# Kernel tuning notes

Hardware: AMD Instinct MI355X
Metric: run time of the kernel (lower is better)

The kernel has to match this reference:

```python
import jax, jax.numpy as jnp
import numpy as np

N = 100_000   # nodes
D = 128       # in_channels
H = 128       # hidden_channels
O = 128       # out_channels
M = 3_200_000 # adjacency nnz (avg degree 32)
E = 200_000   # query edges
P = 500_000   # common-neighbor pairs (padded, all valid here)
COS_EPS = 1e-8
DEG_EPS = 1e-6


def setup_inputs() -> dict:
    key = jax.random.key(0)
    ks = jax.random.split(key, 12)
    x = jax.random.normal(ks[0], (N, D), jnp.float32)
    adj_row = jnp.sort(jax.random.randint(ks[1], (M,), 0, N, jnp.int32))
    adj_col = jax.random.randint(ks[2], (M,), 0, N, jnp.int32)
    edges = jax.random.randint(ks[3], (2, E), 0, N, jnp.int32)
    cn_edge_idx = jnp.sort(jax.random.randint(ks[4], (P,), 0, E, jnp.int32))
    cn_node = jax.random.randint(ks[5], (P,), 0, N, jnp.int32)
    cn_valid = jnp.ones((P,), jnp.bool_)
    # MLP params (Kaiming-ish scale)
    W1 = jax.random.normal(ks[6], (D, H), jnp.float32) / np.sqrt(D)
    b1 = jnp.zeros((H,), jnp.float32)
    W2 = jax.random.normal(ks[7], (H, H), jnp.float32) / np.sqrt(H)
    b2 = jnp.zeros((H,), jnp.float32)
    W3 = jax.random.normal(ks[8], (H, O), jnp.float32) / np.sqrt(H)
    b3 = jnp.zeros((O,), jnp.float32)
    return dict(x=x, adj_row=adj_row, adj_col=adj_col, edges=edges,
                cn_edge_idx=cn_edge_idx, cn_node=cn_node, cn_valid=cn_valid,
                W1=W1, b1=b1, W2=W2, b2=b2, W3=W3, b3=b3)


def _cosine(a, b):
    # torch.nn.CosineSimilarity: dot / max(||a||*||b||, eps)
    dot = jnp.sum(a * b, axis=-1)
    na = jnp.sqrt(jnp.sum(a * a, axis=-1))
    nb = jnp.sqrt(jnp.sum(b * b, axis=-1))
    return dot / jnp.maximum(na * nb, COS_EPS)


def reference(x, adj_row, adj_col, edges, cn_edge_idx, cn_node, cn_valid,
              W1, b1, W2, b2, W3, b3):
    # degrees = adj.sum(-1) + 1e-6 (binary adjacency values)
    ones = jnp.ones(adj_row.shape[0], x.dtype)
    deg = jax.ops.segment_sum(ones, adj_row, num_segments=N) + DEG_EPS
    # x = x + (adj @ x) / deg[:, None]
    agg = jax.ops.segment_sum(x[adj_col], adj_row, num_segments=N)
    h = x + agg / deg[:, None]
    # MLP (BatchNorms are unused in the original forward; dropout = inference)
    h = jax.nn.relu(h @ W1 + b1)
    h = jax.nn.relu(h @ W2 + b2)
    h = h @ W3 + b3                      # [N, O]
    # gather per common-neighbor pair: u = edges[0][e], v = edges[1][e], c = neighbor
    u = edges[0][cn_edge_idx]
    v = edges[1][cn_edge_idx]
    hu, hv, hc = h[u], h[v], h[cn_node]  # [P, O] each
    w = _cosine(hu, hc) * _cosine(hv, hc)
    w = jnp.where(cn_valid, w, jnp.zeros((), h.dtype))
    # sparse row-sum over neighbors per query edge
    scores = jax.ops.segment_sum(w, cn_edge_idx, num_segments=E)
    return jax.nn.sigmoid(scores)
```

## Files before the change

kernel.cpp:

```cpp
#include <hip/hip_runtime.h>
#include <math.h>

constexpr int N_NODES = 100000;
constexpr int DIM     = 128;
constexpr int M_NNZ   = 3200000;
constexpr int E_EDGES = 200000;
constexpr int P_PAIRS = 500000;
constexpr int W_ELEMS = 3 * DIM * DIM;

typedef _Float16 half8  __attribute__((ext_vector_type(8)));
typedef _Float16 half4t __attribute__((ext_vector_type(4)));
typedef _Float16 half2t __attribute__((ext_vector_type(2)));
typedef float    f32x4  __attribute__((ext_vector_type(4)));
typedef float    f32x2  __attribute__((ext_vector_type(2)));
typedef unsigned int u32x2 __attribute__((ext_vector_type(2)));

#if defined(__has_builtin)
#  if __has_builtin(__builtin_amdgcn_cvt_scalef32_pk8_f16_fp8)
#    define HAVE_PK8 1
#  endif
#endif
#ifndef HAVE_PK8
#  define HAVE_PK8 0
#endif

__device__ inline half8 fp8x8_to_h8(u32x2 d) {
#if HAVE_PK8
    return __builtin_amdgcn_cvt_scalef32_pk8_f16_fp8(d, 1.0f);
#else
    f32x2 p0 = __builtin_amdgcn_cvt_pk_f32_fp8(d[0], false);
    f32x2 p1 = __builtin_amdgcn_cvt_pk_f32_fp8(d[0], true);
    f32x2 p2 = __builtin_amdgcn_cvt_pk_f32_fp8(d[1], false);
    f32x2 p3 = __builtin_amdgcn_cvt_pk_f32_fp8(d[1], true);
    return half8{(_Float16)p0[0], (_Float16)p0[1], (_Float16)p1[0], (_Float16)p1[1],
                 (_Float16)p2[0], (_Float16)p2[1], (_Float16)p3[0], (_Float16)p3[1]};
#endif
}

__device__ inline void stage_weight(const _Float16* __restrict__ src,
                                    _Float16* __restrict__ dst) {
    const int tid = threadIdx.x;
    #pragma unroll
    for (int j = 0; j < 8; ++j) {
        const int gg  = j * 256 + tid;
        const int row = gg >> 4, g = gg & 15;
        *(half8*)(dst + (row << 7) + ((g ^ (row & 15)) << 3)) =
            *(const half8*)(src + gg * 8);
    }
}

__device__ inline half8 ldsw(const _Float16* __restrict__ w,
                             int row, int q, int t, int l16) {
    return *(const half8*)(w + (row << 7) + (((q + 4 * t) ^ l16) << 3));
}

__global__ void prep_kernel(
    const float* __restrict__ W1, const float* __restrict__ W2,
    const float* __restrict__ W3, _Float16* __restrict__ Wt,
    const int* __restrict__ adj_row, int* __restrict__ rs, int* __restrict__ re,
    float* __restrict__ out) {
    const int tid = blockIdx.x * blockDim.x + threadIdx.x;
    if (tid < W_ELEMS) {
        int m = tid >> 14, n = (tid >> 7) & 127, k = tid & 127;
        const float* W = (m == 0) ? W1 : (m == 1) ? W2 : W3;
        Wt[tid] = (_Float16)W[k * DIM + n];
        return;
    }
    if (tid < W_ELEMS + M_NNZ) {
        const int p = tid - W_ELEMS;
        const int v = adj_row[p];
        if (p == 0) {
            rs[v] = 0;
            for (int w = 0; w < v; ++w) { rs[w] = 0; re[w] = 0; }
        } else {
            int pv = adj_row[p - 1];
            if (pv != v) {
                re[pv] = p; rs[v] = p;
                for (int w = pv + 1; w < v; ++w) { rs[w] = p; re[w] = p; }
            }
        }
        if (p == M_NNZ - 1) {
            re[v] = M_NNZ;
            for (int w = v + 1; w < N_NODES; ++w) { rs[w] = M_NNZ; re[w] = M_NNZ; }
        }
        return;
    }
    if (tid < W_ELEMS + M_NNZ + E_EDGES) {
        out[tid - W_ELEMS - M_NNZ] = 0.f;
    }
}

__global__ __launch_bounds__(256) void gemm1_kernel(
    const float* __restrict__ x, const _Float16* __restrict__ Wt,
    _Float16* __restrict__ y, unsigned char* __restrict__ y8) {
    __shared__ __align__(16) _Float16 lw[16384];
    const int lane = threadIdx.x & 63;
    const int wave = threadIdx.x >> 6;
    const int q = lane >> 4, l16 = lane & 15;
    const int rBase = blockIdx.x * 128 + wave * 32;

    const int row0 = rBase + l16, row1 = rBase + 16 + l16;
    const int r0 = min(row0, N_NODES - 1), r1 = min(row1, N_NODES - 1);
    const float* Ap0 = x + (size_t)r0 * DIM + q * 8;
    const float* Ap1 = x + (size_t)r1 * DIM + q * 8;
    half8 a0[4], a1[4];
    #pragma unroll
    for (int t = 0; t < 4; ++t) {
        float4 u0 = *(const float4*)(Ap0 + t * 32);
        float4 u1 = *(const float4*)(Ap0 + t * 32 + 4);
        float4 w0 = *(const float4*)(Ap1 + t * 32);
        float4 w1 = *(const float4*)(Ap1 + t * 32 + 4);
        a0[t] = half8{(_Float16)u0.x, (_Float16)u0.y, (_Float16)u0.z, (_Float16)u0.w,
                      (_Float16)u1.x, (_Float16)u1.y, (_Float16)u1.z, (_Float16)u1.w};
        a1[t] = half8{(_Float16)w0.x, (_Float16)w0.y, (_Float16)w0.z, (_Float16)w0.w,
                      (_Float16)w1.x, (_Float16)w1.y, (_Float16)w1.z, (_Float16)w1.w};
    }
    stage_weight(Wt, lw);
    __syncthreads();

    #pragma unroll
    for (int c = 0; c < 8; ++c) {
        f32x4 acc0 = {0.f, 0.f, 0.f, 0.f}, acc1 = {0.f, 0.f, 0.f, 0.f};
        #pragma unroll
        for (int t = 0; t < 4; ++t) {
            const half8 w = ldsw(lw, c * 16 + l16, q, t, l16);
            acc0 = __builtin_amdgcn_mfma_f32_16x16x32_f16(w, a0[t], acc0, 0, 0, 0);
            acc1 = __builtin_amdgcn_mfma_f32_16x16x32_f16(w, a1[t], acc1, 0, 0, 0);
        }
        const int colBase = c * 16 + q * 4;
        half4t o0 = { (_Float16)acc0[0], (_Float16)acc0[1], (_Float16)acc0[2], (_Float16)acc0[3] };
        half4t o1 = { (_Float16)acc1[0], (_Float16)acc1[1], (_Float16)acc1[2], (_Float16)acc1[3] };
        int p0 = __builtin_amdgcn_cvt_pk_fp8_f32(acc0[0], acc0[1], 0, false);
        p0     = __builtin_amdgcn_cvt_pk_fp8_f32(acc0[2], acc0[3], p0, true);
        int p1 = __builtin_amdgcn_cvt_pk_fp8_f32(acc1[0], acc1[1], 0, false);
        p1     = __builtin_amdgcn_cvt_pk_fp8_f32(acc1[2], acc1[3], p1, true);
        if (row0 < N_NODES) {
            *(half4t*)(y + (size_t)row0 * DIM + colBase) = o0;
            *(int*)(y8 + (size_t)row0 * DIM + colBase) = p0;
        }
        if (row1 < N_NODES) {
            *(half4t*)(y + (size_t)row1 * DIM + colBase) = o1;
            *(int*)(y8 + (size_t)row1 * DIM + colBase) = p1;
        }
    }
}

__global__ __launch_bounds__(256) void agg_kernel(
    const _Float16* __restrict__ y, const unsigned char* __restrict__ y8,
    const int* __restrict__ rs, const int* __restrict__ re,
    const int* __restrict__ adj_col, const float* __restrict__ b1,
    _Float16* __restrict__ h1, int node_base) {
    const int wave = threadIdx.x >> 6, lane = threadIdx.x & 63;
    const int node = node_base + blockIdx.x * 4 + wave;
    const int start = rs[node], cnt = re[node] - start;
    const int g = lane >> 4;
    const int l16 = lane & 15;
    const unsigned b8 = (unsigned)l16 * 8;

    float fa[8];
    half8 a0 = {}, a1 = {}, a2 = {}, a3 = {};
    for (int base = 0; base < cnt; base += 64) {
        const int chunk = min(64, cnt - base);
        const int colreg = adj_col[start + base + min(lane, chunk - 1)];
        int j = 0;
        for (; j + 16 <= chunk; j += 16) {
            int cc[4];
            #pragma unroll
            for (int s = 0; s < 4; ++s) cc[s] = __shfl(colreg, j + 4 * s + g);
            u32x2 dv[4];
            #pragma unroll
            for (int s = 0; s < 4; ++s)
                dv[s] = *(const u32x2*)(y8 + (((unsigned)cc[s] << 7) + b8));
            a0 += fp8x8_to_h8(dv[0]);
            a1 += fp8x8_to_h8(dv[1]);
            a2 += fp8x8_to_h8(dv[2]);
            a3 += fp8x8_to_h8(dv[3]);
        }
        for (; j < chunk; j += 4) {
            const int idx = j + g;
            const int c = __shfl(colreg, min(idx, chunk - 1));
            const u32x2 d = *(const u32x2*)(y8 + (((unsigned)c << 7) + b8));
            const half8 v = fp8x8_to_h8(d);
            if (idx < chunk) a0 += v;
        }
    }
    const half8 hs = (a0 + a1) + (a2 + a3);
    #pragma unroll
    for (int t = 0; t < 8; ++t) fa[t] = (float)hs[t];

    #pragma unroll
    for (int t = 0; t < 8; ++t) {
        float f = fa[t];
        f += __shfl_xor(f, 16);
        f += __shfl_xor(f, 32);
        fa[t] = f;
    }
    if (g == 0) {
        const float inv = 1.f / ((float)cnt + 1e-6f);
        const half8 sf = *(const half8*)(y + (size_t)node * DIM + b8);
        const float4 bb0 = *(const float4*)(b1 + b8);
        const float4 bb1 = *(const float4*)(b1 + b8 + 4);
        half8 o;
        #pragma unroll
        for (int t = 0; t < 8; ++t) {
            const float bb = (t < 4) ? ((const float*)&bb0)[t] : ((const float*)&bb1)[t - 4];
            o[t] = (_Float16)fmaxf((float)sf[t] + fa[t] * inv + bb, 0.f);
        }
        *(half8*)(h1 + (size_t)node * DIM + b8) = o;
    }
}

__global__ __launch_bounds__(256) void mlp23_kernel(
    const _Float16* __restrict__ h1, const _Float16* __restrict__ Wt,
    const float* __restrict__ b2, const float* __restrict__ b3,
    unsigned char* __restrict__ hN8) {
    __shared__ __align__(16) _Float16 lw[16384];
    __shared__ __align__(16) _Float16 tile[4][16][136];
    const int lane = threadIdx.x & 63;
    const int wave = threadIdx.x >> 6;
    const int q = lane >> 4, l16 = lane & 15;
    const int node = blockIdx.x * 64 + wave * 16 + l16;
    const int nl = min(node, N_NODES - 1);

    half8 aF[4];
    #pragma unroll
    for (int t = 0; t < 4; ++t)
        aF[t] = *(const half8*)(h1 + (size_t)nl * DIM + q * 8 + t * 32);

    stage_weight(Wt + 16384, lw);
    __syncthreads();

    half4t o2[8];
    #pragma unroll
    for (int c = 0; c < 8; ++c) {
        f32x4 acc = {0.f, 0.f, 0.f, 0.f};
        #pragma unroll
        for (int t = 0; t < 4; ++t) {
            const half8 w = ldsw(lw, c * 16 + l16, q, t, l16);
            acc = __builtin_amdgcn_mfma_f32_16x16x32_f16(w, aF[t], acc, 0, 0, 0);
        }
        const int colBase = c * 16 + q * 4;
        const float4 bb = *(const float4*)(b2 + colBase);
        o2[c] = half4t{ (_Float16)fmaxf(acc[0] + bb.x, 0.f),
                        (_Float16)fmaxf(acc[1] + bb.y, 0.f),
                        (_Float16)fmaxf(acc[2] + bb.z, 0.f),
                        (_Float16)fmaxf(acc[3] + bb.w, 0.f) };
    }
    __syncthreads();

    stage_weight(Wt + 32768, lw);

    #pragma unroll
    for (int c = 0; c < 8; ++c)
        *(half4t*)(&tile[wave][l16][c * 16 + q * 4]) = o2[c];
    #pragma unroll
    for (int t = 0; t < 4; ++t)
        aF[t] = *(const half8*)(&tile[wave][l16][q * 8 + t * 32]);

    __syncthreads();

    f32x4 vals[8];
    float s = 0.f;
    #pragma unroll
    for (int c = 0; c < 8; ++c) {
        f32x4 acc = {0.f, 0.f, 0.f, 0.f};
        #pragma unroll
        for (int t = 0; t < 4; ++t) {
            const half8 w = ldsw(lw, c * 16 + l16, q, t, l16);
            acc = __builtin_amdgcn_mfma_f32_16x16x32_f16(w, aF[t], acc, 0, 0, 0);
        }
        const int colBase = c * 16 + q * 4;
        const float4 bb = *(const float4*)(b3 + colBase);
        f32x4 v;
        v[0] = acc[0] + bb.x; v[1] = acc[1] + bb.y;
        v[2] = acc[2] + bb.z; v[3] = acc[3] + bb.w;
        s += v[0]*v[0] + v[1]*v[1] + v[2]*v[2] + v[3]*v[3];
        vals[c] = v;
    }
    s += __shfl_xor(s, 16);
    s += __shfl_xor(s, 32);
    const float rn = 1.f / fmaxf(sqrtf(s), 1e-4f);
    if (node < N_NODES) {
        #pragma unroll
        for (int c = 0; c < 8; ++c) {
            const int colBase = c * 16 + q * 4;
            int pk = __builtin_amdgcn_cvt_pk_fp8_f32(vals[c][0] * rn, vals[c][1] * rn, 0, false);
            pk     = __builtin_amdgcn_cvt_pk_fp8_f32(vals[c][2] * rn, vals[c][3] * rn, pk, true);
            *(int*)(hN8 + (((unsigned)node << 7) + colBase)) = pk;
        }
    }
}

__global__ __launch_bounds__(256) void edge_pair_kernel(
    const unsigned char* __restrict__ h8,
    const int* __restrict__ edges, const int* __restrict__ cn_edge,
    const int* __restrict__ cn_node, float* __restrict__ scores) {
    const int lane = threadIdx.x & 63;
    const int wave = threadIdx.x >> 6;
    const int g = lane >> 4, l16 = lane & 15;
    const int p = blockIdx.x * 16 + wave * 4 + g;
    const unsigned e8 = (unsigned)l16 * 8;

    const int e = cn_edge[p];
    const int c = cn_node[p];
    const int u = edges[e], v = edges[E_EDGES + e];
    const half8 hc = fp8x8_to_h8(*(const u32x2*)(h8 + (((unsigned)c << 7) + e8)));
    const half8 hu = fp8x8_to_h8(*(const u32x2*)(h8 + (((unsigned)u << 7) + e8)));
    const half8 hv = fp8x8_to_h8(*(const u32x2*)(h8 + (((unsigned)v << 7) + e8)));
    float du = 0.f, dv = 0.f;
    #pragma unroll
    for (int t = 0; t < 4; ++t) {
        const half2t a = half2t{hc[2 * t], hc[2 * t + 1]};
        du = __builtin_amdgcn_fdot2(half2t{hu[2 * t], hu[2 * t + 1]}, a, du, false);
        dv = __builtin_amdgcn_fdot2(half2t{hv[2 * t], hv[2 * t + 1]}, a, dv, false);
    }
    #pragma unroll
    for (int off = 1; off < 16; off <<= 1) {
        du += __shfl_xor(du, off);
        dv += __shfl_xor(dv, off);
    }
    if (l16 == 0) atomicAdd(scores + e, du * dv);
}

__global__ void sigmoid_kernel(float* __restrict__ out) {
    const int e = blockIdx.x * blockDim.x + threadIdx.x;
    if (e < E_EDGES) out[e] = 1.f / (1.f + expf(-out[e]));
}

extern "C" void kernel_launch(void* const* d_in, const int* in_sizes, int n_in,
                              void* d_out, int out_size, void* d_ws, size_t ws_size,
                              hipStream_t stream) {
    const float* x     = (const float*)d_in[0];
    const int* adj_row = (const int*)d_in[1];
    const int* adj_col = (const int*)d_in[2];
    const int* edges   = (const int*)d_in[3];
    const int* cn_edge = (const int*)d_in[4];
    const int* cn_node = (const int*)d_in[5];
    const float* W1 = (const float*)d_in[7];
    const float* b1 = (const float*)d_in[8];
    const float* W2 = (const float*)d_in[9];
    const float* b2 = (const float*)d_in[10];
    const float* W3 = (const float*)d_in[11];
    const float* b3 = (const float*)d_in[12];
    float* out = (float*)d_out;

    char* base = (char*)d_ws;
    _Float16* y  = (_Float16*)base;
    _Float16* h1 = (_Float16*)(base + 25600000);
    unsigned char* y8 = (unsigned char*)(base + 51200000);
    unsigned char* hN8 = y8;
    _Float16* Wt = (_Float16*)(base + 64000000);
    int* rs = (int*)(base + 64098304);
    int* re = (int*)(base + 64498304);

    const int prep_threads = W_ELEMS + M_NNZ + E_EDGES;
    prep_kernel<<<(prep_threads + 255) / 256, 256, 0, stream>>>(
        W1, W2, W3, Wt, adj_row, rs, re, out);

    gemm1_kernel<<<(N_NODES + 127) / 128, 256, 0, stream>>>(x, Wt, y, y8);
    agg_kernel<<<N_NODES / 8, 256, 0, stream>>>(y, y8, rs, re, adj_col, b1, h1, 0);
    agg_kernel<<<N_NODES / 8, 256, 0, stream>>>(y, y8, rs, re, adj_col, b1, h1, N_NODES / 2);
    mlp23_kernel<<<(N_NODES + 63) / 64, 256, 0, stream>>>(h1, Wt, b2, b3, hN8);
    edge_pair_kernel<<<P_PAIRS / 16, 256, 0, stream>>>(hN8, edges, cn_edge, cn_node, out);
    sigmoid_kernel<<<(E_EDGES + 255) / 256, 256, 0, stream>>>(out);
}
```

Measured before the change: 287.2 us.

## Compute edge-pair dot products with MFMA and split aggregation into four launches

The edge-pair kernel now gives each lane one pair and uses 16x16x32 f16 MFMA to compute hu·hc and hv·hc. Only the diagonal of the 16x16 result is used, which replaces the per-lane fdot2 and 16-lane shuffle reduction, and each wave now covers 16 pairs instead of 4. Most of each MFMA's output is wasted, and the gathered row loads are now strided across lanes. Aggregation is split into four launches over quarter ranges instead of two, which presumably changes cache locality for the gathered rows.

```diff
diff --git a/kernel.cpp b/kernel.cpp
--- a/kernel.cpp
+++ b/kernel.cpp
@@ -297,29 +297,30 @@
     const int* __restrict__ cn_node, float* __restrict__ scores) {
     const int lane = threadIdx.x & 63;
     const int wave = threadIdx.x >> 6;
-    const int g = lane >> 4, l16 = lane & 15;
-    const int p = blockIdx.x * 16 + wave * 4 + g;
-    const unsigned e8 = (unsigned)l16 * 8;
-
-    const int e = cn_edge[p];
-    const int c = cn_node[p];
+    const int q = lane >> 4, l16 = lane & 15;
+    const int pbase = (blockIdx.x * 4 + wave) * 16;
+    const int p = pbase + l16;
+    const int pc = min(p, P_PAIRS - 1);
+
+    const int e = cn_edge[pc];
+    const int c = cn_node[pc];
     const int u = edges[e], v = edges[E_EDGES + e];
-    const half8 hc = fp8x8_to_h8(*(const u32x2*)(h8 + (((unsigned)c << 7) + e8)));
-    const half8 hu = fp8x8_to_h8(*(const u32x2*)(h8 + (((unsigned)u << 7) + e8)));
-    const half8 hv = fp8x8_to_h8(*(const u32x2*)(h8 + (((unsigned)v << 7) + e8)));
-    float du = 0.f, dv = 0.f;
+    const unsigned off0 = (unsigned)q * 8;
+
+    f32x4 au = {0.f, 0.f, 0.f, 0.f}, av = {0.f, 0.f, 0.f, 0.f};
     #pragma unroll
     for (int t = 0; t < 4; ++t) {
-        const half2t a = half2t{hc[2 * t], hc[2 * t + 1]};
-        du = __builtin_amdgcn_fdot2(half2t{hu[2 * t], hu[2 * t + 1]}, a, du, false);
-        dv = __builtin_amdgcn_fdot2(half2t{hv[2 * t], hv[2 * t + 1]}, a, dv, false);
-    }
-    #pragma unroll
-    for (int off = 1; off < 16; off <<= 1) {
-        du += __shfl_xor(du, off);
-        dv += __shfl_xor(dv, off);
-    }
-    if (l16 == 0) atomicAdd(scores + e, du * dv);
+        const unsigned off = off0 + t * 32;
+        const half8 hc = fp8x8_to_h8(*(const u32x2*)(h8 + (((unsigned)c << 7) + off)));
+        const half8 hu = fp8x8_to_h8(*(const u32x2*)(h8 + (((unsigned)u << 7) + off)));
+        const half8 hv = fp8x8_to_h8(*(const u32x2*)(h8 + (((unsigned)v << 7) + off)));
+        au = __builtin_amdgcn_mfma_f32_16x16x32_f16(hu, hc, au, 0, 0, 0);
+        av = __builtin_amdgcn_mfma_f32_16x16x32_f16(hv, hc, av, 0, 0, 0);
+    }
+    if ((l16 >> 2) == q && p < P_PAIRS) {
+        const int i = l16 & 3;
+        atomicAdd(scores + e, au[i] * av[i]);
+    }
 }
 
 __global__ void sigmoid_kernel(float* __restrict__ out) {
@@ -358,9 +359,11 @@
         W1, W2, W3, Wt, adj_row, rs, re, out);
 
     gemm1_kernel<<<(N_NODES + 127) / 128, 256, 0, stream>>>(x, Wt, y, y8);
-    agg_kernel<<<N_NODES / 8, 256, 0, stream>>>(y, y8, rs, re, adj_col, b1, h1, 0);
-    agg_kernel<<<N_NODES / 8, 256, 0, stream>>>(y, y8, rs, re, adj_col, b1, h1, N_NODES / 2);
+    agg_kernel<<<N_NODES / 16, 256, 0, stream>>>(y, y8, rs, re, adj_col, b1, h1, 0);
+    agg_kernel<<<N_NODES / 16, 256, 0, stream>>>(y, y8, rs, re, adj_col, b1, h1, 25000);
+    agg_kernel<<<N_NODES / 16, 256, 0, stream>>>(y, y8, rs, re, adj_col, b1, h1, 50000);
+    agg_kernel<<<N_NODES / 16, 256, 0, stream>>>(y, y8, rs, re, adj_col, b1, h1, 75000);
     mlp23_kernel<<<(N_NODES + 63) / 64, 256, 0, stream>>>(h1, Wt, b2, b3, hN8);
-    edge_pair_kernel<<<P_PAIRS / 16, 256, 0, stream>>>(hN8, edges, cn_edge, cn_node, out);
+    edge_pair_kernel<<<(P_PAIRS + 63) / 64, 256, 0, stream>>>(hN8, edges, cn_edge, cn_node, out);
     sigmoid_kernel<<<(E_EDGES + 255) / 256, 256, 0, stream>>>(out);
 }
```

After: 292.6 us. No clear change (+1.9%).
